# Performance work log

Hardware: AMD Instinct MI355X
Metric: run time of the kernel (lower is better)

Reference implementation:

```python
import jax, jax.numpy as jnp
import numpy as np

B, TA, TB, DIN, DEMB = 32, 128, 1024, 1280, 512
LN_EPS = 1e-5
MM_EPS = 1e-6


def _param(key, shape, scale=0.02):
    return (jax.random.normal(key, shape, dtype=jnp.float32) * scale)


def setup_inputs() -> dict:
    key = jax.random.key(0)
    ks = jax.random.split(key, 24)
    inp = {
        'pep_esm': jax.random.normal(ks[0], (B, TA, DIN), dtype=jnp.float32),
        'rec_esm': jax.random.normal(ks[1], (B, TB, DIN), dtype=jnp.float32),
        'pep_mask': jax.random.randint(ks[2], (B, TA), 0, 2, dtype=jnp.int32),
        'rec_mask': jax.random.randint(ks[3], (B, TB), 0, 2, dtype=jnp.int32),
        'temperature': jnp.asarray(1.0, dtype=jnp.float32),
    }
    i = 4
    for pre in ('pep', 'rec'):
        inp[pre + '_pw'] = _param(ks[i], (DIN, DEMB)); i += 1
        inp[pre + '_pb'] = jnp.zeros((DEMB,), jnp.float32)
        inp[pre + '_f1w'] = _param(ks[i], (DEMB, DEMB)); i += 1
        inp[pre + '_f1b'] = jnp.zeros((DEMB,), jnp.float32)
        inp[pre + '_lng'] = jnp.ones((DEMB,), jnp.float32)
        inp[pre + '_lnb'] = jnp.zeros((DEMB,), jnp.float32)
        inp[pre + '_f2w'] = _param(ks[i], (DEMB, DEMB)); i += 1
        inp[pre + '_f2b'] = jnp.zeros((DEMB,), jnp.float32)
    return inp


def _encode(x, pw, pb, f1w, f1b, lng, lnb, f2w, f2b):
    # projection -> (Linear, ReLU, LayerNorm) -> final Linear (dropout=0 at eval)
    e = x @ pw + pb                                   # [b, t, DEMB]
    h = jax.nn.relu(e @ f1w + f1b)
    mu = h.mean(-1, keepdims=True)
    var = ((h - mu) ** 2).mean(-1, keepdims=True)
    h = (h - mu) * jax.lax.rsqrt(var + LN_EPS) * lng + lnb
    out = h @ f2w + f2b
    return out / jnp.linalg.norm(out, axis=-1, keepdims=True)


def _masked_mean(t, mask, axis=-1):
    numer = jnp.where(mask, t, 0.0).sum(axis=axis)
    denom = jnp.maximum(mask.sum(axis=axis).astype(t.dtype), MM_EPS)
    return numer / denom


def reference(pep_esm, rec_esm, pep_mask, rec_mask, temperature,
              pep_pw, pep_pb, pep_f1w, pep_f1b, pep_lng, pep_lnb, pep_f2w, pep_f2b,
              rec_pw, rec_pb, rec_f1w, rec_f1b, rec_lng, rec_lnb, rec_f2w, rec_f2b):
    hA = _encode(pep_esm, pep_pw, pep_pb, pep_f1w, pep_f1b, pep_lng, pep_lnb, pep_f2w, pep_f2b)
    hB = _encode(rec_esm, rec_pw, rec_pb, rec_f1w, rec_f1b, rec_lng, rec_lnb, rec_f2w, rec_f2b)
    mA = pep_mask.astype(bool)                        # [bA, tA]
    mB = rec_mask.astype(bool)                        # [bB, tB]
    # pairwise token similarity: [bA, bB, tA, tB]
    sim = jnp.einsum('atd,bsd->abts', hA, hB) / temperature
    cmask = mA[:, None, :, None] & mB[None, :, None, :]
    neg = jnp.finfo(sim.dtype).min
    sim_m = jnp.where(cmask, sim, neg)
    sA = sim_m.max(axis=-1)                            # [bA, bB, tA]
    sB = sim_m.max(axis=-2)                            # [bA, bB, tB]
    sim_scores_A = _masked_mean(sA, mA[:, None, :])    # [bA, bB]
    sim_scores_B = _masked_mean(sB, mB[None, :, :])    # [bA, bB]
    return sim_scores_A, sim_scores_B
```

## Files before the change

### kernel.cpp

```cpp
#include <hip/hip_runtime.h>
#include <float.h>
#include <stddef.h>
#include <stdint.h>

#define DIN_   1280
#define DEMB_  512
#define NBAT_  32
#define TA_    128
#define TB_    1024
#define LN_EPS_ 1e-5f

using short8  = __attribute__((ext_vector_type(8))) short;
using ushort8 = __attribute__((ext_vector_type(8))) unsigned short;
using f32x4   = __attribute__((ext_vector_type(4))) float;

typedef const __attribute__((address_space(1))) unsigned int gu32;
typedef __attribute__((address_space(3))) unsigned int lu32;

__device__ __forceinline__ void gld_lds16(const void* g, void* l) {
    __builtin_amdgcn_global_load_lds((gu32*)g, (lu32*)l, 16, 0, 0);
}

__device__ __forceinline__ unsigned short f2bf(float x) {
    unsigned u = __float_as_uint(x);
    u += 0x7FFFu + ((u >> 16) & 1u);
    return (unsigned short)(u >> 16);
}
__device__ __forceinline__ float bf2f(unsigned short u) {
    return __uint_as_float((unsigned)u << 16);
}
__device__ __forceinline__ int clampi(int v, int hi) {
    return v < 0 ? 0 : (v > hi ? hi : v);
}

__global__ __launch_bounds__(64) void compact_idx_kernel(
    const int* __restrict__ mask, int T, int* __restrict__ idx, int* __restrict__ cnt)
{
    const int b = blockIdx.x, lane = threadIdx.x;
    const int base = b * T;
    int run = 0;
    for (int c = 0; c < T; c += 64) {
        int m = mask[base + c + lane] != 0;
        unsigned long long bal = __ballot(m);
        int pos = run + __popcll(bal & ((1ull << lane) - 1ull));
        idx[base + c + lane] = m ? pos : -1;
        run += __popcll(bal);
    }
    if (lane == 0) cnt[b] = run;
}

__global__ __launch_bounds__(64) void offsets_kernel(
    const int* __restrict__ cntA, const int* __restrict__ cntB,
    int* __restrict__ offA, int* __restrict__ offB, int* __restrict__ tot)
{
    if (threadIdx.x == 0) {
        int s = 0;
        for (int i = 0; i < NBAT_; ++i) { offA[i] = s; s += cntA[i]; }
        tot[0] = s;
        s = 0;
        for (int i = 0; i < NBAT_; ++i) { offB[i] = s; s += cntB[i]; }
        tot[1] = s;
    }
}

__global__ __launch_bounds__(256) void srcrows_kernel(
    const int* __restrict__ idx, const int* __restrict__ off, int shift,
    int* __restrict__ srcrows)
{
    int r = blockIdx.x * 256 + threadIdx.x;
    int d = idx[r];
    if (d >= 0) srcrows[off[r >> shift] + d] = r;
}

struct WPack { const float* src[4]; unsigned short* dst[4]; };
__global__ __launch_bounds__(256) void wtrans_multi_kernel(WPack p, int K, int N)
{
    __shared__ float tile[32][33];
    const float* W = p.src[blockIdx.z];
    unsigned short* Wt = p.dst[blockIdx.z];
    const int k0 = blockIdx.x * 32, n0 = blockIdx.y * 32;
    const int r = threadIdx.x >> 5, c = threadIdx.x & 31;
    #pragma unroll
    for (int i = 0; i < 4; ++i)
        tile[r + i * 8][c] = W[(size_t)(k0 + r + i * 8) * N + n0 + c];
    __syncthreads();
    #pragma unroll
    for (int i = 0; i < 4; ++i)
        Wt[(size_t)(n0 + r + i * 8) * K + k0 + c] = f2bf(tile[c][r + i * 8]);
}

template<int K, bool RELU>
__global__ __launch_bounds__(512, 4) void egemm_bf16(
    const unsigned short* __restrict__ A, const unsigned short* __restrict__ Wt,
    const float* __restrict__ bias, unsigned short* __restrict__ C,
    const int* __restrict__ Nrp)
{
    const int bid = blockIdx.x;
    const int row0 = (bid >> 2) * 128, col0 = (bid & 3) * 128;
    if (row0 >= *Nrp) return;
    __shared__ __align__(16) unsigned char Abuf[128 * 64 * 2];
    __shared__ __align__(16) unsigned char Bbuf[128 * 64 * 2];
    const int t = threadIdx.x;
    const int wave = t >> 6, lane = t & 63;
    const int wr = wave >> 2, wc = wave & 3;
    const int cl = lane & 15, rg = lane >> 4;

    const int pr0 = t >> 3, pq0 = t & 7;
    const int pr1 = pr0 + 64;
    const int ks0 = ((pq0 ^ (pr0 & 7)) * 8);
    const int ks1 = ((pq0 ^ (pr1 & 7)) * 8);
    const unsigned short* Aglob = A + (size_t)row0 * K;
    const unsigned short* Bglob = Wt + (size_t)col0 * K;

    int aoff[4], asw[4], boff[2], bsw[2];
    #pragma unroll
    for (int m = 0; m < 4; ++m) {
        int r = wr * 64 + m * 16 + cl;
        aoff[m] = r * 128; asw[m] = (r & 7) << 4;
    }
    #pragma unroll
    for (int n = 0; n < 2; ++n) {
        int c = wc * 32 + n * 16 + cl;
        boff[n] = c * 128; bsw[n] = (c & 7) << 4;
    }

    f32x4 acc[4][2];
    #pragma unroll
    for (int m = 0; m < 4; ++m) {
        acc[m][0] = (f32x4){0.f, 0.f, 0.f, 0.f};
        acc[m][1] = (f32x4){0.f, 0.f, 0.f, 0.f};
    }
    for (int k0 = 0; k0 < K; k0 += 64) {
        gld_lds16(Aglob + (size_t)pr0 * K + k0 + ks0, Abuf + t * 16);
        gld_lds16(Aglob + (size_t)pr1 * K + k0 + ks1, Abuf + (t + 512) * 16);
        gld_lds16(Bglob + (size_t)pr0 * K + k0 + ks0, Bbuf + t * 16);
        gld_lds16(Bglob + (size_t)pr1 * K + k0 + ks1, Bbuf + (t + 512) * 16);
        __syncthreads();
        #pragma unroll
        for (int h = 0; h < 2; ++h) {
            const int cb = h * 64 + rg * 16;
            short8 av[4], bv[2];
            #pragma unroll
            for (int m = 0; m < 4; ++m)
                av[m] = *(const short8*)(Abuf + aoff[m] + (cb ^ asw[m]));
            #pragma unroll
            for (int n = 0; n < 2; ++n)
                bv[n] = *(const short8*)(Bbuf + boff[n] + (cb ^ bsw[n]));
            #pragma unroll
            for (int m = 0; m < 4; ++m)
                #pragma unroll
                for (int n = 0; n < 2; ++n)
                    acc[m][n] = __builtin_amdgcn_mfma_f32_16x16x32_bf16(
                        av[m], bv[n], acc[m][n], 0, 0, 0);
        }
        __syncthreads();
    }
    const float b0 = bias[col0 + wc * 32 + cl];
    const float b1 = bias[col0 + wc * 32 + 16 + cl];
    #pragma unroll
    for (int m = 0; m < 4; ++m)
        #pragma unroll
        for (int j = 0; j < 4; ++j) {
            int row = row0 + wr * 64 + m * 16 + rg * 4 + j;
            float v0 = acc[m][0][j] + b0;
            float v1 = acc[m][1][j] + b1;
            if (RELU) { v0 = fmaxf(v0, 0.f); v1 = fmaxf(v1, 0.f); }
            C[(size_t)row * DEMB_ + col0 + wc * 32 + cl]      = f2bf(v0);
            C[(size_t)row * DEMB_ + col0 + wc * 32 + 16 + cl] = f2bf(v1);
        }
}

template<int K, bool RELU>
__global__ __launch_bounds__(512, 4) void egemm_f32a_g(
    const float* __restrict__ A, const unsigned short* __restrict__ Wt,
    const float* __restrict__ bias, unsigned short* __restrict__ C,
    const int* __restrict__ srcrows, const int* __restrict__ Nrp, int Mmax)
{
    const int bid = blockIdx.x;
    const int row0 = (bid >> 2) * 128, col0 = (bid & 3) * 128;
    if (row0 >= *Nrp) return;
    __shared__ __align__(16) unsigned char Abuf[128 * 64 * 2];
    __shared__ __align__(16) unsigned char Bbuf[128 * 64 * 2];
    const int t = threadIdx.x;
    const int wave = t >> 6, lane = t & 63;
    const int wr = wave >> 2, wc = wave & 3;
    const int cl = lane & 15, rg = lane >> 4;

    const int pr0 = t >> 3, pq0 = t & 7;
    const int pr1 = pr0 + 64;
    const int ks0 = ((pq0 ^ (pr0 & 7)) * 8);
    const int ks1 = ((pq0 ^ (pr1 & 7)) * 8);
    const int ad0 = pr0 * 128 + ((pq0 ^ (pr0 & 7)) << 4);
    const int ad1 = pr1 * 128 + ((pq0 ^ (pr1 & 7)) << 4);
    const int sr0 = clampi(srcrows[row0 + pr0], Mmax - 1);
    const int sr1 = clampi(srcrows[row0 + pr1], Mmax - 1);
    const float* Ar0 = A + (size_t)sr0 * K;
    const float* Ar1 = A + (size_t)sr1 * K;
    const unsigned short* Bglob = Wt + (size_t)col0 * K;

    int aoff[4], asw[4], boff[2], bsw[2];
    #pragma unroll
    for (int m = 0; m < 4; ++m) {
        int r = wr * 64 + m * 16 + cl;
        aoff[m] = r * 128; asw[m] = (r & 7) << 4;
    }
    #pragma unroll
    for (int n = 0; n < 2; ++n) {
        int c = wc * 32 + n * 16 + cl;
        boff[n] = c * 128; bsw[n] = (c & 7) << 4;
    }

    f32x4 acc[4][2];
    #pragma unroll
    for (int m = 0; m < 4; ++m) {
        acc[m][0] = (f32x4){0.f, 0.f, 0.f, 0.f};
        acc[m][1] = (f32x4){0.f, 0.f, 0.f, 0.f};
    }
    for (int k0 = 0; k0 < K; k0 += 64) {
        gld_lds16(Bglob + (size_t)pr0 * K + k0 + ks0, Bbuf + t * 16);
        gld_lds16(Bglob + (size_t)pr1 * K + k0 + ks1, Bbuf + (t + 512) * 16);
        {
            const float* s0 = Ar0 + k0 + pq0 * 8;
            const float* s1 = Ar1 + k0 + pq0 * 8;
            float4 u0 = *(const float4*)(s0), u1 = *(const float4*)(s0 + 4);
            float4 u2 = *(const float4*)(s1), u3 = *(const float4*)(s1 + 4);
            ushort8 w0, w1;
            w0[0] = f2bf(u0.x); w0[1] = f2bf(u0.y); w0[2] = f2bf(u0.z); w0[3] = f2bf(u0.w);
            w0[4] = f2bf(u1.x); w0[5] = f2bf(u1.y); w0[6] = f2bf(u1.z); w0[7] = f2bf(u1.w);
            w1[0] = f2bf(u2.x); w1[1] = f2bf(u2.y); w1[2] = f2bf(u2.z); w1[3] = f2bf(u2.w);
            w1[4] = f2bf(u3.x); w1[5] = f2bf(u3.y); w1[6] = f2bf(u3.z); w1[7] = f2bf(u3.w);
            *(ushort8*)(Abuf + ad0) = w0;
            *(ushort8*)(Abuf + ad1) = w1;
        }
        __syncthreads();
        #pragma unroll
        for (int h = 0; h < 2; ++h) {
            const int cb = h * 64 + rg * 16;
            short8 av[4], bv[2];
            #pragma unroll
            for (int m = 0; m < 4; ++m)
                av[m] = *(const short8*)(Abuf + aoff[m] + (cb ^ asw[m]));
            #pragma unroll
            for (int n = 0; n < 2; ++n)
                bv[n] = *(const short8*)(Bbuf + boff[n] + (cb ^ bsw[n]));
            #pragma unroll
            for (int m = 0; m < 4; ++m)
                #pragma unroll
                for (int n = 0; n < 2; ++n)
                    acc[m][n] = __builtin_amdgcn_mfma_f32_16x16x32_bf16(
                        av[m], bv[n], acc[m][n], 0, 0, 0);
        }
        __syncthreads();
    }
    const float b0 = bias[col0 + wc * 32 + cl];
    const float b1 = bias[col0 + wc * 32 + 16 + cl];
    #pragma unroll
    for (int m = 0; m < 4; ++m)
        #pragma unroll
        for (int j = 0; j < 4; ++j) {
            int row = row0 + wr * 64 + m * 16 + rg * 4 + j;
            float v0 = acc[m][0][j] + b0;
            float v1 = acc[m][1][j] + b1;
            if (RELU) { v0 = fmaxf(v0, 0.f); v1 = fmaxf(v1, 0.f); }
            C[(size_t)row * DEMB_ + col0 + wc * 32 + cl]      = f2bf(v0);
            C[(size_t)row * DEMB_ + col0 + wc * 32 + 16 + cl] = f2bf(v1);
        }
}

__global__ __launch_bounds__(256) void ln_bf16_kernel(
    unsigned short* __restrict__ h, const float* __restrict__ g, const float* __restrict__ b,
    const int* __restrict__ Nrp)
{
    const int lane = threadIdx.x & 63;
    const int row = blockIdx.x * 4 + (threadIdx.x >> 6);
    if (row >= *Nrp) return;
    unsigned short* p = h + (size_t)row * DEMB_;
    ushort8 v = *(const ushort8*)(p + lane * 8);
    float x[8];
    #pragma unroll
    for (int i = 0; i < 8; ++i) x[i] = bf2f(v[i]);
    float s = 0.f;
    #pragma unroll
    for (int i = 0; i < 8; ++i) s += x[i];
    #pragma unroll
    for (int d = 32; d >= 1; d >>= 1) s += __shfl_xor(s, d);
    float mu = s * (1.f / DEMB_);
    float sq = 0.f;
    #pragma unroll
    for (int i = 0; i < 8; ++i) { float dd = x[i] - mu; sq += dd * dd; }
    #pragma unroll
    for (int d = 32; d >= 1; d >>= 1) sq += __shfl_xor(sq, d);
    float rs = 1.f / sqrtf(sq * (1.f / DEMB_) + LN_EPS_);
    float4 g0 = *(const float4*)(g + lane * 8);
    float4 g1 = *(const float4*)(g + lane * 8 + 4);
    float4 b0 = *(const float4*)(b + lane * 8);
    float4 b1 = *(const float4*)(b + lane * 8 + 4);
    float gg[8] = {g0.x, g0.y, g0.z, g0.w, g1.x, g1.y, g1.z, g1.w};
    float bb[8] = {b0.x, b0.y, b0.z, b0.w, b1.x, b1.y, b1.z, b1.w};
    ushort8 o;
    #pragma unroll
    for (int i = 0; i < 8; ++i) o[i] = f2bf((x[i] - mu) * rs * gg[i] + bb[i]);
    *(ushort8*)(p + lane * 8) = o;
}

__global__ __launch_bounds__(256) void l2norm_bf16_kernel(
    const unsigned short* __restrict__ h, unsigned short* __restrict__ o,
    const int* __restrict__ Nrp)
{
    const int lane = threadIdx.x & 63;
    const int row = blockIdx.x * 4 + (threadIdx.x >> 6);
    if (row >= *Nrp) return;
    const unsigned short* p = h + (size_t)row * DEMB_;
    ushort8 v = *(const ushort8*)(p + lane * 8);
    float x[8];
    #pragma unroll
    for (int i = 0; i < 8; ++i) x[i] = bf2f(v[i]);
    float sq = 0.f;
    #pragma unroll
    for (int i = 0; i < 8; ++i) sq += x[i] * x[i];
    #pragma unroll
    for (int d = 32; d >= 1; d >>= 1) sq += __shfl_xor(sq, d);
    float rs = 1.f / sqrtf(sq);
    ushort8 w;
    #pragma unroll
    for (int i = 0; i < 8; ++i) w[i] = f2bf(x[i] * rs);
    *(ushort8*)(o + (size_t)row * DEMB_ + lane * 8) = w;
}

__global__ __launch_bounds__(128, 3) void sim_part_kernel(
    const unsigned short* __restrict__ hA,
    const unsigned short* __restrict__ hB,
    const int* __restrict__ offA, const int* __restrict__ cntA,
    const int* __restrict__ offB, const int* __restrict__ cntB,
    const float* __restrict__ temp,
    float* __restrict__ rowmax_ws,
    float* __restrict__ colmax_ws)
{
    __shared__ __align__(16) unsigned char Abuf[64 * 64 * 2];
    __shared__ __align__(16) unsigned char Bbuf[128 * 64 * 2];
    __shared__ float rowpart[2][64];

    const int bid = blockIdx.x;
    const int g = (bid & 7) * 2048 + (bid >> 3);
    const int b = g >> 9;
    const int a = (g >> 4) & 31;
    const int at = (g >> 3) & 1, a0 = at << 6;
    const int s0t = g & 7, s0 = s0t << 7;

    const int nBb = cntB[b];
    if (s0 >= nBb) return;
    const int nAa = cntA[a];
    if (a0 >= nAa) return;

    const int t = threadIdx.x;
    const int w = t >> 6, lane = t & 63;
    const int cl = lane & 15, rg = lane >> 4;
    const float invT = 1.0f / temp[0];

    const int pr = t >> 3, pq = t & 7;
    const int ks = (pq ^ (pr & 7)) * 8;
    const int abase = offA[a] + a0 + pr;
    const int bbase = offB[b] + s0 + pr;
    const unsigned short* Ap[4];
    const unsigned short* Bp[8];
    #pragma unroll
    for (int i = 0; i < 4; ++i)
        Ap[i] = hA + (size_t)clampi(abase + 16 * i, NBAT_ * TA_ - 1) * DEMB_ + ks;
    #pragma unroll
    for (int i = 0; i < 8; ++i)
        Bp[i] = hB + (size_t)clampi(bbase + 16 * i, NBAT_ * TB_ - 1) * DEMB_ + ks;

    unsigned mabits = 0;
    #pragma unroll
    for (int m = 0; m < 4; ++m)
        #pragma unroll
        for (int j = 0; j < 4; ++j)
            if (a0 + m * 16 + rg * 4 + j < nAa) mabits |= 1u << (m * 4 + j);
    int mb[4];
    #pragma unroll
    for (int n = 0; n < 4; ++n)
        mb[n] = (s0 + w * 64 + n * 16 + cl) < nBb;

    int aoff[4], asw[4], boff[4], bsw[4];
    #pragma unroll
    for (int m = 0; m < 4; ++m) {
        int r = m * 16 + cl;
        aoff[m] = r * 128; asw[m] = (r & 7) << 4;
    }
    #pragma unroll
    for (int n = 0; n < 4; ++n) {
        int c = w * 64 + n * 16 + cl;
        boff[n] = c * 128; bsw[n] = (c & 7) << 4;
    }

    f32x4 acc[4][4];
    #pragma unroll
    for (int m = 0; m < 4; ++m)
        #pragma unroll
        for (int n = 0; n < 4; ++n)
            acc[m][n] = (f32x4){0.f, 0.f, 0.f, 0.f};

    for (int k0 = 0; k0 < DEMB_; k0 += 64) {
        #pragma unroll
        for (int i = 0; i < 4; ++i)
            gld_lds16(Ap[i] + k0, Abuf + (t + 128 * i) * 16);
        #pragma unroll
        for (int i = 0; i < 8; ++i)
            gld_lds16(Bp[i] + k0, Bbuf + (t + 128 * i) * 16);
        __syncthreads();
        #pragma unroll
        for (int h = 0; h < 2; ++h) {
            const int cb = h * 64 + rg * 16;
            short8 av[4], bv[4];
            #pragma unroll
            for (int m = 0; m < 4; ++m)
                av[m] = *(const short8*)(Abuf + aoff[m] + (cb ^ asw[m]));
            #pragma unroll
            for (int n = 0; n < 4; ++n)
                bv[n] = *(const short8*)(Bbuf + boff[n] + (cb ^ bsw[n]));
            #pragma unroll
            for (int m = 0; m < 4; ++m)
                #pragma unroll
                for (int n = 0; n < 4; ++n)
                    acc[m][n] = __builtin_amdgcn_mfma_f32_16x16x32_bf16(
                        av[m], bv[n], acc[m][n], 0, 0, 0);
        }
        __syncthreads();
    }
    float rmax[4][4];
    float cmax[4] = {-FLT_MAX, -FLT_MAX, -FLT_MAX, -FLT_MAX};
    #pragma unroll
    for (int m = 0; m < 4; ++m)
        #pragma unroll
        for (int j = 0; j < 4; ++j) {
            const bool ra = (mabits >> (m * 4 + j)) & 1;
            float rm = -FLT_MAX;
            #pragma unroll
            for (int n = 0; n < 4; ++n) {
                float v = (ra && mb[n]) ? acc[m][n][j] * invT : -FLT_MAX;
                rm = fmaxf(rm, v);
                cmax[n] = fmaxf(cmax[n], v);
            }
            rmax[m][j] = rm;
        }
    #pragma unroll
    for (int d = 1; d < 16; d <<= 1)
        #pragma unroll
        for (int m = 0; m < 4; ++m)
            #pragma unroll
            for (int j = 0; j < 4; ++j)
                rmax[m][j] = fmaxf(rmax[m][j], __shfl_xor(rmax[m][j], d));
    if (cl == 0) {
        #pragma unroll
        for (int m = 0; m < 4; ++m)
            #pragma unroll
            for (int j = 0; j < 4; ++j)
                rowpart[w][m * 16 + rg * 4 + j] = rmax[m][j];
    }
    #pragma unroll
    for (int n = 0; n < 4; ++n) {
        cmax[n] = fmaxf(cmax[n], __shfl_xor(cmax[n], 16));
        cmax[n] = fmaxf(cmax[n], __shfl_xor(cmax[n], 32));
    }
    if (rg == 0) {
        float* cw = colmax_ws + ((size_t)((a * NBAT_ + b) * 2 + at)) * TB_ + s0;
        #pragma unroll
        for (int n = 0; n < 4; ++n)
            cw[w * 64 + n * 16 + cl] = cmax[n];
    }
    __syncthreads();
    if (t < 64) {
        float r = fmaxf(rowpart[0][t], rowpart[1][t]);
        rowmax_ws[(((size_t)(a * NBAT_ + b)) * 8 + s0t) * 128 + a0 + t] = r;
    }
}

__global__ __launch_bounds__(256) void sim_reduce_kernel(
    const float* __restrict__ rowmax_ws, const float* __restrict__ colmax_ws,
    const int* __restrict__ cntA, const int* __restrict__ cntB,
    float* __restrict__ out)
{
    __shared__ float red[4][2];
    const int bid = blockIdx.x;
    const int a = bid >> 5, b = bid & 31;
    const int t = threadIdx.x, lane = t & 63, wave = t >> 6;
    const int nAa = cntA[a], nBb = cntB[b];
    const int nt = (nBb + 127) >> 7;

    float numA = 0.f, sumB = 0.f;
    if (t < 128 && t < nAa) {
        const float* rp = rowmax_ws + ((size_t)(a * NBAT_ + b)) * 8 * 128 + t;
        float r = -FLT_MAX;
        for (int s = 0; s < nt; ++s) r = fmaxf(r, rp[s * 128]);
        numA = r;
    }
    const float* cp0 = colmax_ws + ((size_t)(a * NBAT_ + b)) * 2 * TB_;
    const float* cp1 = cp0 + TB_;
    const bool two = nAa > 64;
    #pragma unroll
    for (int i = 0; i < 4; ++i) {
        int s = t + i * 256;
        if (s < nBb) {
            float v = cp0[s];
            if (two) v = fmaxf(v, cp1[s]);
            sumB += v;
        }
    }
    #pragma unroll
    for (int d = 32; d >= 1; d >>= 1) {
        numA += __shfl_xor(numA, d);
        sumB += __shfl_xor(sumB, d);
    }
    if (lane == 0) { red[wave][0] = numA; red[wave][1] = sumB; }
    __syncthreads();
    if (t == 0) {
        float n  = red[0][0] + red[1][0] + red[2][0] + red[3][0];
        float nb = red[0][1] + red[1][1] + red[2][1] + red[3][1];
        out[a * NBAT_ + b] = n / fmaxf((float)nAa, 1e-6f);
        out[NBAT_ * NBAT_ + a * NBAT_ + b] = nb / fmaxf((float)nBb, 1e-6f);
    }
}

extern "C" void kernel_launch(void* const* d_in, const int* in_sizes, int n_in,
                              void* d_out, int out_size, void* d_ws, size_t ws_size,
                              hipStream_t stream)
{
    const float* pep_esm  = (const float*)d_in[0];
    const float* rec_esm  = (const float*)d_in[1];
    const int*   pep_mask = (const int*)d_in[2];
    const int*   rec_mask = (const int*)d_in[3];
    const float* temp     = (const float*)d_in[4];
    const float* pep_pw  = (const float*)d_in[5];
    const float* pep_pb  = (const float*)d_in[6];
    const float* pep_f1w = (const float*)d_in[7];
    const float* pep_f1b = (const float*)d_in[8];
    const float* pep_lng = (const float*)d_in[9];
    const float* pep_lnb = (const float*)d_in[10];
    const float* pep_f2w = (const float*)d_in[11];
    const float* pep_f2b = (const float*)d_in[12];
    const float* rec_pw  = (const float*)d_in[13];
    const float* rec_pb  = (const float*)d_in[14];
    const float* rec_f1w = (const float*)d_in[15];
    const float* rec_f1b = (const float*)d_in[16];
    const float* rec_lng = (const float*)d_in[17];
    const float* rec_lnb = (const float*)d_in[18];
    const float* rec_f2w = (const float*)d_in[19];
    const float* rec_f2b = (const float*)d_in[20];
    float* out = (float*)d_out;

    const int Mr = NBAT_ * TB_;
    const int Mp = NBAT_ * TA_;

    char* base = (char*)d_ws;
    unsigned short* R1    = (unsigned short*)(base);
    unsigned short* R2    = (unsigned short*)(base + ((size_t)32 << 20));
    unsigned short* hB_c  = (unsigned short*)(base + ((size_t)64 << 20));
    unsigned short* hA_c  = (unsigned short*)(base + ((size_t)96 << 20));
    unsigned short* wts   = (unsigned short*)(base + ((size_t)101 << 20));
    unsigned short* rec_pwt  = wts;
    unsigned short* pep_pwt  = rec_pwt + 512 * 1280;
    unsigned short* rec_f1wt = pep_pwt + 512 * 1280;
    unsigned short* rec_f2wt = rec_f1wt + 512 * 512;
    unsigned short* pep_f1wt = rec_f2wt + 512 * 512;
    unsigned short* pep_f2wt = pep_f1wt + 512 * 512;
    float* rowmax_ws = (float*)(base + ((size_t)106 << 20));
    float* colmax_ws = (float*)(base + ((size_t)110 << 20));
    int* idxA = (int*)(base + ((size_t)118 << 20));
    int* idxB = idxA + Mp;
    int* cntA = idxB + Mr;
    int* cntB = cntA + NBAT_;
    int* offA = cntB + NBAT_;
    int* offB = offA + NBAT_;
    int* tot  = offB + NBAT_;
    int* srcA = tot + 2;
    int* srcB = srcA + Mp;

    dim3 b256(256);
    compact_idx_kernel<<<dim3(NBAT_), dim3(64), 0, stream>>>(pep_mask, TA_, idxA, cntA);
    compact_idx_kernel<<<dim3(NBAT_), dim3(64), 0, stream>>>(rec_mask, TB_, idxB, cntB);
    offsets_kernel<<<dim3(1), dim3(64), 0, stream>>>(cntA, cntB, offA, offB, tot);
    srcrows_kernel<<<dim3(Mp / 256), b256, 0, stream>>>(idxA, offA, 7, srcA);
    srcrows_kernel<<<dim3(Mr / 256), b256, 0, stream>>>(idxB, offB, 10, srcB);

    {
        WPack p1; p1.src[0] = rec_pw; p1.dst[0] = rec_pwt;
                  p1.src[1] = pep_pw; p1.dst[1] = pep_pwt;
                  p1.src[2] = rec_pw; p1.dst[2] = rec_pwt;
                  p1.src[3] = rec_pw; p1.dst[3] = rec_pwt;
        wtrans_multi_kernel<<<dim3(DIN_ / 32, DEMB_ / 32, 2), b256, 0, stream>>>(p1, DIN_, DEMB_);
        WPack p2; p2.src[0] = rec_f1w; p2.dst[0] = rec_f1wt;
                  p2.src[1] = rec_f2w; p2.dst[1] = rec_f2wt;
                  p2.src[2] = pep_f1w; p2.dst[2] = pep_f1wt;
                  p2.src[3] = pep_f2w; p2.dst[3] = pep_f2wt;
        wtrans_multi_kernel<<<dim3(DEMB_ / 32, DEMB_ / 32, 4), b256, 0, stream>>>(p2, DEMB_, DEMB_);
    }

    int* NrA = tot;
    int* NrB = tot + 1;
    egemm_f32a_g<DIN_, false><<<dim3((Mr / 128) * 4), dim3(512), 0, stream>>>(rec_esm, rec_pwt, rec_pb, R1, srcB, NrB, Mr);
    egemm_bf16<DEMB_, true><<<dim3((Mr / 128) * 4), dim3(512), 0, stream>>>(R1, rec_f1wt, rec_f1b, R2, NrB);
    ln_bf16_kernel<<<dim3(Mr / 4), b256, 0, stream>>>(R2, rec_lng, rec_lnb, NrB);
    egemm_bf16<DEMB_, false><<<dim3((Mr / 128) * 4), dim3(512), 0, stream>>>(R2, rec_f2wt, rec_f2b, R1, NrB);
    l2norm_bf16_kernel<<<dim3(Mr / 4), b256, 0, stream>>>(R1, hB_c, NrB);
    egemm_f32a_g<DIN_, false><<<dim3((Mp / 128) * 4), dim3(512), 0, stream>>>(pep_esm, pep_pwt, pep_pb, R1, srcA, NrA, Mp);
    egemm_bf16<DEMB_, true><<<dim3((Mp / 128) * 4), dim3(512), 0, stream>>>(R1, pep_f1wt, pep_f1b, R2, NrA);
    ln_bf16_kernel<<<dim3(Mp / 4), b256, 0, stream>>>(R2, pep_lng, pep_lnb, NrA);
    egemm_bf16<DEMB_, false><<<dim3((Mp / 128) * 4), dim3(512), 0, stream>>>(R2, pep_f2wt, pep_f2b, R1, NrA);
    l2norm_bf16_kernel<<<dim3(Mp / 4), b256, 0, stream>>>(R1, hA_c, NrA);
    sim_part_kernel<<<dim3(NBAT_ * NBAT_ * 2 * 8), dim3(128), 0, stream>>>(
        hA_c, hB_c, offA, cntA, offB, cntB, temp, rowmax_ws, colmax_ws);
    sim_reduce_kernel<<<dim3(NBAT_ * NBAT_), b256, 0, stream>>>(
        rowmax_ws, colmax_ws, cntA, cntB, out);
}
```

Measured before the change: 314.5 us.

## Load sim GEMM operands directly from global memory into registers, dropping LDS staging

```diff
diff --git a/kernel.cpp b/kernel.cpp
--- a/kernel.cpp
+++ b/kernel.cpp
@@ -327,7 +327,7 @@
     *(ushort8*)(o + (size_t)row * DEMB_ + lane * 8) = w;
 }
 
-__global__ __launch_bounds__(128, 3) void sim_part_kernel(
+__global__ __launch_bounds__(256, 3) void sim_part_kernel(
     const unsigned short* __restrict__ hA,
     const unsigned short* __restrict__ hB,
     const int* __restrict__ offA, const int* __restrict__ cntA,
@@ -336,39 +336,37 @@
     float* __restrict__ rowmax_ws,
     float* __restrict__ colmax_ws)
 {
-    __shared__ __align__(16) unsigned char Abuf[64 * 64 * 2];
-    __shared__ __align__(16) unsigned char Bbuf[128 * 64 * 2];
-    __shared__ float rowpart[2][64];
-
     const int bid = blockIdx.x;
-    const int g = (bid & 7) * 2048 + (bid >> 3);
-    const int b = g >> 9;
-    const int a = (g >> 4) & 31;
-    const int at = (g >> 3) & 1, a0 = at << 6;
-    const int s0t = g & 7, s0 = s0t << 7;
+    const int g = (bid & 7) * 1024 + (bid >> 3);
+    const int b = g >> 8;
+    const int a = (g >> 3) & 31;
+    const int at = (g >> 2) & 1, a0 = at << 6;
+    const int sq = g & 3;
 
     const int nBb = cntB[b];
-    if (s0 >= nBb) return;
     const int nAa = cntA[a];
-    if (a0 >= nAa) return;
+    if (a0 >= nAa || sq * 256 >= nBb) return;
 
     const int t = threadIdx.x;
     const int w = t >> 6, lane = t & 63;
+    const int s0c = sq * 4 + w, s0 = s0c * 64;
+    if (s0 >= nBb) return;
+
     const int cl = lane & 15, rg = lane >> 4;
     const float invT = 1.0f / temp[0];
 
-    const int pr = t >> 3, pq = t & 7;
-    const int ks = (pq ^ (pr & 7)) * 8;
-    const int abase = offA[a] + a0 + pr;
-    const int bbase = offB[b] + s0 + pr;
-    const unsigned short* Ap[4];
-    const unsigned short* Bp[8];
-    #pragma unroll
-    for (int i = 0; i < 4; ++i)
-        Ap[i] = hA + (size_t)clampi(abase + 16 * i, NBAT_ * TA_ - 1) * DEMB_ + ks;
-    #pragma unroll
-    for (int i = 0; i < 8; ++i)
-        Bp[i] = hB + (size_t)clampi(bbase + 16 * i, NBAT_ * TB_ - 1) * DEMB_ + ks;
+    const unsigned short* Ab[4];
+    const unsigned short* Bb[4];
+    #pragma unroll
+    for (int m = 0; m < 4; ++m) {
+        int r = clampi(offA[a] + a0 + m * 16 + cl, NBAT_ * TA_ - 1);
+        Ab[m] = hA + (size_t)r * DEMB_ + rg * 8;
+    }
+    #pragma unroll
+    for (int n = 0; n < 4; ++n) {
+        int c = clampi(offB[b] + s0 + n * 16 + cl, NBAT_ * TB_ - 1);
+        Bb[n] = hB + (size_t)c * DEMB_ + rg * 8;
+    }
 
     unsigned mabits = 0;
     #pragma unroll
@@ -379,19 +377,7 @@
     int mb[4];
     #pragma unroll
     for (int n = 0; n < 4; ++n)
-        mb[n] = (s0 + w * 64 + n * 16 + cl) < nBb;
-
-    int aoff[4], asw[4], boff[4], bsw[4];
-    #pragma unroll
-    for (int m = 0; m < 4; ++m) {
-        int r = m * 16 + cl;
-        aoff[m] = r * 128; asw[m] = (r & 7) << 4;
-    }
-    #pragma unroll
-    for (int n = 0; n < 4; ++n) {
-        int c = w * 64 + n * 16 + cl;
-        boff[n] = c * 128; bsw[n] = (c & 7) << 4;
-    }
+        mb[n] = (s0 + n * 16 + cl) < nBb;
 
     f32x4 acc[4][4];
     #pragma unroll
@@ -400,33 +386,31 @@
         for (int n = 0; n < 4; ++n)
             acc[m][n] = (f32x4){0.f, 0.f, 0.f, 0.f};
 
-    for (int k0 = 0; k0 < DEMB_; k0 += 64) {
-        #pragma unroll
-        for (int i = 0; i < 4; ++i)
-            gld_lds16(Ap[i] + k0, Abuf + (t + 128 * i) * 16);
-        #pragma unroll
-        for (int i = 0; i < 8; ++i)
-            gld_lds16(Bp[i] + k0, Bbuf + (t + 128 * i) * 16);
-        __syncthreads();
-        #pragma unroll
-        for (int h = 0; h < 2; ++h) {
-            const int cb = h * 64 + rg * 16;
-            short8 av[4], bv[4];
-            #pragma unroll
-            for (int m = 0; m < 4; ++m)
-                av[m] = *(const short8*)(Abuf + aoff[m] + (cb ^ asw[m]));
-            #pragma unroll
-            for (int n = 0; n < 4; ++n)
-                bv[n] = *(const short8*)(Bbuf + boff[n] + (cb ^ bsw[n]));
-            #pragma unroll
-            for (int m = 0; m < 4; ++m)
-                #pragma unroll
-                for (int n = 0; n < 4; ++n)
-                    acc[m][n] = __builtin_amdgcn_mfma_f32_16x16x32_bf16(
-                        av[m], bv[n], acc[m][n], 0, 0, 0);
-        }
-        __syncthreads();
-    }
+    #pragma unroll
+    for (int k = 0; k < 8; ++k) {
+        const int kb = k * 64;
+        short8 av0[4], av1[4], bv0[4], bv1[4];
+        #pragma unroll
+        for (int m = 0; m < 4; ++m) {
+            av0[m] = *(const short8*)(Ab[m] + kb);
+            av1[m] = *(const short8*)(Ab[m] + kb + 32);
+        }
+        #pragma unroll
+        for (int n = 0; n < 4; ++n) {
+            bv0[n] = *(const short8*)(Bb[n] + kb);
+            bv1[n] = *(const short8*)(Bb[n] + kb + 32);
+        }
+        #pragma unroll
+        for (int m = 0; m < 4; ++m)
+            #pragma unroll
+            for (int n = 0; n < 4; ++n) {
+                acc[m][n] = __builtin_amdgcn_mfma_f32_16x16x32_bf16(
+                    av0[m], bv0[n], acc[m][n], 0, 0, 0);
+                acc[m][n] = __builtin_amdgcn_mfma_f32_16x16x32_bf16(
+                    av1[m], bv1[n], acc[m][n], 0, 0, 0);
+            }
+    }
+
     float rmax[4][4];
     float cmax[4] = {-FLT_MAX, -FLT_MAX, -FLT_MAX, -FLT_MAX};
     #pragma unroll
@@ -451,11 +435,12 @@
             for (int j = 0; j < 4; ++j)
                 rmax[m][j] = fmaxf(rmax[m][j], __shfl_xor(rmax[m][j], d));
     if (cl == 0) {
+        float* rw = rowmax_ws + ((size_t)(a * NBAT_ + b) * 16 + s0c) * 128 + a0;
         #pragma unroll
         for (int m = 0; m < 4; ++m)
             #pragma unroll
             for (int j = 0; j < 4; ++j)
-                rowpart[w][m * 16 + rg * 4 + j] = rmax[m][j];
+                rw[m * 16 + rg * 4 + j] = rmax[m][j];
     }
     #pragma unroll
     for (int n = 0; n < 4; ++n) {
@@ -466,12 +451,7 @@
         float* cw = colmax_ws + ((size_t)((a * NBAT_ + b) * 2 + at)) * TB_ + s0;
         #pragma unroll
         for (int n = 0; n < 4; ++n)
-            cw[w * 64 + n * 16 + cl] = cmax[n];
-    }
-    __syncthreads();
-    if (t < 64) {
-        float r = fmaxf(rowpart[0][t], rowpart[1][t]);
-        rowmax_ws[(((size_t)(a * NBAT_ + b)) * 8 + s0t) * 128 + a0 + t] = r;
+            cw[n * 16 + cl] = cmax[n];
     }
 }
 
@@ -485,11 +465,11 @@
     const int a = bid >> 5, b = bid & 31;
     const int t = threadIdx.x, lane = t & 63, wave = t >> 6;
     const int nAa = cntA[a], nBb = cntB[b];
-    const int nt = (nBb + 127) >> 7;
+    const int nt = (nBb + 63) >> 6;
 
     float numA = 0.f, sumB = 0.f;
     if (t < 128 && t < nAa) {
-        const float* rp = rowmax_ws + ((size_t)(a * NBAT_ + b)) * 8 * 128 + t;
+        const float* rp = rowmax_ws + (size_t)(a * NBAT_ + b) * 16 * 128 + t;
         float r = -FLT_MAX;
         for (int s = 0; s < nt; ++s) r = fmaxf(r, rp[s * 128]);
         numA = r;
@@ -563,9 +543,9 @@
     unsigned short* rec_f2wt = rec_f1wt + 512 * 512;
     unsigned short* pep_f1wt = rec_f2wt + 512 * 512;
     unsigned short* pep_f2wt = pep_f1wt + 512 * 512;
-    float* rowmax_ws = (float*)(base + ((size_t)106 << 20));
-    float* colmax_ws = (float*)(base + ((size_t)110 << 20));
-    int* idxA = (int*)(base + ((size_t)118 << 20));
+    float* rowmax_ws = (float*)(base);
+    float* colmax_ws = (float*)(base + ((size_t)8 << 20));
+    int* idxA = (int*)(base + ((size_t)106 << 20));
     int* idxB = idxA + Mp;
     int* cntA = idxB + Mr;
     int* cntB = cntA + NBAT_;
@@ -607,7 +587,7 @@
     ln_bf16_kernel<<<dim3(Mp / 4), b256, 0, stream>>>(R2, pep_lng, pep_lnb, NrA);
     egemm_bf16<DEMB_, false><<<dim3((Mp / 128) * 4), dim3(512), 0, stream>>>(R2, pep_f2wt, pep_f2b, R1, NrA);
     l2norm_bf16_kernel<<<dim3(Mp / 4), b256, 0, stream>>>(R1, hA_c, NrA);
-    sim_part_kernel<<<dim3(NBAT_ * NBAT_ * 2 * 8), dim3(128), 0, stream>>>(
+    sim_part_kernel<<<dim3(NBAT_ * NBAT_ * 2 * 4), b256, 0, stream>>>(
         hA_c, hB_c, offA, cntA, offB, cntB, temp, rowmax_ws, colmax_ws);
     sim_reduce_kernel<<<dim3(NBAT_ * NBAT_), b256, 0, stream>>>(
         rowmax_ws, colmax_ws, cntA, cntB, out);
```

Result: slower. 544.7 us (+73.2%).
